# Kernel optimization log

Measured on AMD Instinct MI355X. Metric: run time of the kernel, lower is better.

## Reference

```python
import jax, jax.numpy as jnp
import numpy as np

N = 50000      # nodes
E = 800000     # edges
F = 500        # num_features
HID = 64       # hidden_channels
H = 4          # num_heads
HC = HID // H  # headc = 16
C = 8          # num_classes
KHOP = 2       # K hops
CST = 1e-5


def setup_inputs() -> dict:
    key = jax.random.key(0)
    ks = jax.random.split(key, 12)
    s = 0.02
    return {
        "node_feat": jax.random.normal(ks[0], (N, F), dtype=jnp.float32),
        "edge_index": jax.random.randint(ks[1], (2, E), 0, N, dtype=jnp.int64),
        "Wi": jax.random.normal(ks[2], (F, HID), dtype=jnp.float32) * s,
        "bi": jnp.zeros((HID,), dtype=jnp.float32),
        "Wq": jax.random.normal(ks[3], (HID, H * HC), dtype=jnp.float32) * s,
        "bq": jnp.zeros((H * HC,), dtype=jnp.float32),
        "Wk": jax.random.normal(ks[4], (HID, H * HC), dtype=jnp.float32) * s,
        "bk": jnp.zeros((H * HC,), dtype=jnp.float32),
        "Wv": jax.random.normal(ks[5], (HID, H * C), dtype=jnp.float32) * s,
        "bv": jnp.zeros((H * C,), dtype=jnp.float32),
        "Wo": jax.random.normal(ks[6], (H * C, C), dtype=jnp.float32) * s,
        "bo": jnp.zeros((C,), dtype=jnp.float32),
        "hopwise": jnp.ones((KHOP + 1,), dtype=jnp.float32),
        "headwise": jnp.zeros((H, KHOP), dtype=jnp.float32),
        "teleport": jnp.ones((1,), dtype=jnp.float32),
    }


def reference(node_feat, edge_index, Wi, bi, Wq, bq, Wk, bk, Wv, bv, Wo, bo,
              hopwise, headwise, teleport):
    row, col = edge_index[0], edge_index[1]
    # degree(col): in-degree; norm = deg^-1 indexed at row (as in the torch code)
    deg = jax.ops.segment_sum(jnp.ones((E,), dtype=node_feat.dtype), col,
                              num_segments=N)
    deg_inv = jnp.where(deg > 0, 1.0 / deg, 0.0)  # [N]

    x = jax.nn.relu(node_feat @ Wi + bi)          # dropout p=0.0 / eval -> identity
    Q = (1.0 + jax.nn.elu(x @ Wq + bq)).reshape(N, H, HC)
    Kf = (1.0 + jax.nn.elu(x @ Wk + bk)).reshape(N, H, HC)
    V = (x @ Wv + bv).reshape(N, H, C)

    M = jnp.einsum('nhi,nhj->nhij', Kf, V)        # [N,H,HC,C]
    hidden = V * hopwise[0]                       # ind_gamma & gamma_softmax
    layerwise = jax.nn.softmax(headwise, axis=0)  # softmax over heads (dim=-2)

    # global attention (teleport) term
    teleportM = jnp.sum(M, axis=0, keepdims=True) / N      # [1,H,HC,C]
    teleportK = jnp.sum(Kf, axis=0, keepdims=True) / N     # [1,H,HC]
    teleportH = jnp.einsum('nhi,bhij->nhj', Q, teleportM)  # [N,H,C]
    teleportC = jnp.einsum('nhi,bhi->nh', Q, teleportK)[..., None] + CST
    teleportH = (teleportH / teleportC).sum(axis=-2)       # [N,C]

    for hop in range(KHOP):
        # norm[e] = deg_inv[row[e]]  =>  pre-scale source nodes, then scatter-add
        M = jax.ops.segment_sum((M * deg_inv[:, None, None, None])[row], col,
                                num_segments=N)
        Kf = jax.ops.segment_sum((Kf * deg_inv[:, None, None])[row], col,
                                 num_segments=N)
        Hh = jnp.einsum('nhi,nhij->nhj', Q, M)             # [N,H,C]
        Cc = jnp.einsum('nhi,nhi->nh', Q, Kf)[..., None] + CST
        gamma = hopwise[hop + 1] * layerwise[:, hop][:, None]  # [H,1]
        hidden = hidden + gamma * (Hh / Cc)

    # multi_concat output projection
    hidden = hidden.reshape(N, H * C) @ Wo + bo
    return hidden + teleport * teleportH
```

## Files before the change

kernel.cpp:

```cpp
#include <hip/hip_runtime.h>
#include <hip/hip_bf16.h>
#include <stdint.h>
#include <stddef.h>

#define NN 50000
#define NE 800000
#define FIN 500
#define HIDN 64
#define NH 4
#define HCD 16
#define NC 8
#define KVROW 192
#define CSTF 1e-5f
#define SCAN_NB 196
#define XBLKS 3125

typedef float f32x2 __attribute__((ext_vector_type(2)));
typedef __attribute__((ext_vector_type(8))) short bf16x8;
typedef __attribute__((ext_vector_type(4))) float f32x4;

__device__ inline float bf_lo(unsigned u) {
    union { unsigned i; float f; } v; v.i = u << 16; return v.f;
}
__device__ inline f32x2 bfpair(unsigned u) {
    union { unsigned i; float f; } lo, hi;
    lo.i = u << 16; hi.i = u & 0xffff0000u;
    f32x2 r; r.x = lo.f; r.y = hi.f; return r;
}
__device__ inline unsigned short f2bf(float f) {
    union { float f; unsigned i; } v; v.f = f;
    unsigned r = v.i + 0x7fffu + ((v.i >> 16) & 1u);
    return (unsigned short)(r >> 16);
}
__device__ inline unsigned pack2bf(float a, float b) {
    __hip_bfloat162 h = __float22bfloat162_rn(make_float2(a, b));
    unsigned r; __builtin_memcpy(&r, &h, 4); return r;
}


__global__ void k_deg_wt(const int* __restrict__ col, int* __restrict__ deg,
                         const float* __restrict__ Wi, unsigned short* __restrict__ Wt) {
    int e = blockIdx.x * blockDim.x + threadIdx.x;
    if (e < NE) atomicAdd(&deg[col[e]], 1);
    if (e < 64 * 512) {
        int c = e >> 9;
        int k = e & 511;
        Wt[e] = (k < FIN) ? f2bf(Wi[(size_t)k * 64 + c]) : (unsigned short)0;
    }
}


__global__ void k_bsum(const int* __restrict__ deg, int* __restrict__ bsum,
                       float* __restrict__ dinv, int* __restrict__ cursor,
                       float* __restrict__ tMK) {
    __shared__ int red[256];
    int b = blockIdx.x, t = threadIdx.x;
    int i = b * 256 + t;
    int d = (i < NN) ? deg[i] : 0;
    if (i < NN) {
        dinv[i] = d > 0 ? 1.0f / (float)d : 0.0f;
        cursor[i] = 0;
    }
    if (b == 0)
        for (int j = t; j < 576; j += 256) tMK[j] = 0.f;
    red[t] = d;
    __syncthreads();
    for (int s = 128; s > 0; s >>= 1) {
        if (t < s) red[t] += red[t + s];
        __syncthreads();
    }
    if (t == 0) bsum[b] = red[0];
}

__global__ void k_bscan(const int* __restrict__ bsum, int* __restrict__ bex) {
    __shared__ int s[256];
    int t = threadIdx.x;
    int own = (t < SCAN_NB) ? bsum[t] : 0;
    s[t] = own;
    __syncthreads();
    for (int d = 1; d < 256; d <<= 1) {
        int v = (t >= d) ? s[t - d] : 0;
        __syncthreads();
        s[t] += v;
        __syncthreads();
    }
    if (t < SCAN_NB) bex[t] = s[t] - own;
}

__global__ void k_expand(const int* __restrict__ deg, const int* __restrict__ bex,
                         int* __restrict__ offs) {
    __shared__ int s[256];
    int b = blockIdx.x, t = threadIdx.x;
    int i = b * 256 + t;
    int v = (i < NN) ? deg[i] : 0;
    s[t] = v;
    __syncthreads();
    for (int d = 1; d < 256; d <<= 1) {
        int a = (t >= d) ? s[t - d] : 0;
        __syncthreads();
        s[t] += a;
        __syncthreads();
    }
    int excl = s[t] - v + bex[b];
    if (i < NN) offs[i] = excl;
    if (i == NN - 1) offs[NN] = excl + v;
}

__global__ void k_scatter(const int* __restrict__ row, const int* __restrict__ col,
                          const int* __restrict__ offs, int* __restrict__ cursor,
                          int* __restrict__ csr_src) {
    int e = blockIdx.x * blockDim.x + threadIdx.x;
    if (e < NE) {
        int c = col[e];
        int pos = offs[c] + atomicAdd(&cursor[c], 1);
        csr_src[pos] = row[e];
    }
}


__global__ __launch_bounds__(256) void k_xgemm(const float* __restrict__ nf,
                                               const unsigned short* __restrict__ Wt,
                                               const float* __restrict__ bi,
                                               float* __restrict__ x) {
    __shared__ __align__(16) float atile[16 * 516];
    int t = threadIdx.x;
    int lane = t & 63;
    int w = t >> 6;
    int quad = lane >> 4;
    int l15 = lane & 15;
    int n0 = blockIdx.x * 16;

#pragma unroll
    for (int i = 0; i < 4; i++) {
        int r = w * 4 + i;
        const float* rp = nf + (size_t)(n0 + r) * FIN;
        float4 v0 = *(const float4*)(rp + 4 * lane);
        int c1 = 256 + 4 * lane;
        int c1c = c1 > 496 ? 496 : c1;
        float4 v1 = *(const float4*)(rp + c1c);
        *(float4*)&atile[r * 516 + 4 * lane] = v0;
        *(float4*)&atile[r * 516 + c1] = v1;
    }
    __syncthreads();

    int kbase = w * 128;
    f32x4 acc[4];
#pragma unroll
    for (int ct = 0; ct < 4; ct++) acc[ct] = (f32x4){0.f, 0.f, 0.f, 0.f};

#pragma unroll
    for (int ks = 0; ks < 4; ks++) {
        int kk = kbase + ks * 32 + quad * 8;
        f32x4 fa = *(const f32x4*)&atile[l15 * 516 + kk];
        f32x4 fb = *(const f32x4*)&atile[l15 * 516 + kk + 4];
        union { unsigned u[4]; bf16x8 v; } A;
        A.u[0] = pack2bf(fa.x, fa.y); A.u[1] = pack2bf(fa.z, fa.w);
        A.u[2] = pack2bf(fb.x, fb.y); A.u[3] = pack2bf(fb.z, fb.w);
#pragma unroll
        for (int ct = 0; ct < 4; ct++) {
            bf16x8 b = *(const bf16x8*)&Wt[(size_t)(ct * 16 + l15) * 512 + kk];
            acc[ct] = __builtin_amdgcn_mfma_f32_16x16x32_bf16(A.v, b, acc[ct], 0, 0, 0);
        }
    }
    __syncthreads();

    float* red = atile;
#pragma unroll
    for (int ct = 0; ct < 4; ct++)
#pragma unroll
        for (int r = 0; r < 4; r++)
            red[(w * 16 + quad * 4 + r) * 68 + ct * 16 + l15] = acc[ct][r];
    __syncthreads();

    int ocol = t & 63;
    int orow0 = t >> 6;
    float bv = bi[ocol];
#pragma unroll
    for (int i = 0; i < 4; i++) {
        int orow = i * 4 + orow0;
        float s = red[(0 * 16 + orow) * 68 + ocol] + red[(1 * 16 + orow) * 68 + ocol]
                + red[(2 * 16 + orow) * 68 + ocol] + red[(3 * 16 + orow) * 68 + ocol];
        x[(size_t)(n0 + orow) * 64 + ocol] = fmaxf(s + bv, 0.f);
    }
}


__global__ __launch_bounds__(256) void k_qkv(const float* __restrict__ x,
    const float* __restrict__ Wq, const float* __restrict__ bq,
    const float* __restrict__ Wk, const float* __restrict__ bk,
    const float* __restrict__ Wv, const float* __restrict__ bv,
    const float* __restrict__ hopwise, const float* __restrict__ dinv,
    float* __restrict__ Qg, float* __restrict__ hid,
    unsigned char* __restrict__ kv0, float* __restrict__ tMK) {
    __shared__ float wq_s[64 * 64], wk_s[64 * 64], wv_s[64 * 32];
    __shared__ float bq_s[64], bk_s[64], bv_s[32];
    __shared__ float xs[4][8][64];
    __shared__ float tacc[576];
    int t = threadIdx.x;
    for (int i = t; i < 4096; i += 256) { wq_s[i] = Wq[i]; wk_s[i] = Wk[i]; }
    for (int i = t; i < 2048; i += 256) wv_s[i] = Wv[i];
    if (t < 64) { bq_s[t] = bq[t]; bk_s[t] = bk[t]; }
    if (t >= 64 && t < 96) bv_s[t - 64] = bv[t - 64];
    for (int i = t; i < 576; i += 256) tacc[i] = 0.f;
    __syncthreads();
    int lane = t & 63;
    int w = t >> 6;
    int h = lane >> 4;
    int vcol = lane & 31;
    float hw0 = hopwise[0];
    float tkp = 0.f;
    float tmp_[8];
#pragma unroll
    for (int j = 0; j < 8; j++) tmp_[j] = 0.f;
    int tiles = (NN + 31) >> 5;
    for (int tile = blockIdx.x; tile < tiles; tile += gridDim.x) {
        int n0 = tile * 32 + w * 8;
        __syncthreads();
#pragma unroll
        for (int u = 0; u < 8; u++) {
            int n = n0 + u;
            xs[w][u][lane] = (n < NN) ? x[(size_t)n * 64 + lane] : 0.f;
        }
        __syncthreads();
        float aq[8], ak[8], av[8];
#pragma unroll
        for (int u = 0; u < 8; u++) { aq[u] = 0.f; ak[u] = 0.f; av[u] = 0.f; }
        for (int f = 0; f < 64; f++) {
            float wqv = wq_s[f * 64 + lane];
            float wkv = wk_s[f * 64 + lane];
            float wvv = wv_s[f * 32 + vcol];
#pragma unroll
            for (int u = 0; u < 8; u++) {
                float xf = xs[w][u][f];
                aq[u] = fmaf(xf, wqv, aq[u]);
                ak[u] = fmaf(xf, wkv, ak[u]);
                av[u] = fmaf(xf, wvv, av[u]);
            }
        }
#pragma unroll
        for (int u = 0; u < 8; u++) {
            int n = n0 + u;
            float q = aq[u] + bq_s[lane];
            float k = ak[u] + bk_s[lane];
            float v = av[u] + bv_s[vcol];
            float Qv = q > 0.f ? 1.f + q : expf(q);
            float Kv = k > 0.f ? 1.f + k : expf(k);
            if (n < NN) {
                Qg[(size_t)n * 64 + lane] = Qv;
                float vj[8];
#pragma unroll
                for (int j = 0; j < 8; j++) vj[j] = __shfl(v, h * 8 + j, 64);
                tkp += Kv;
#pragma unroll
                for (int j = 0; j < 8; j++) tmp_[j] += Kv * vj[j];
                float dv = dinv[n];
                unsigned short* kvrow = (unsigned short*)(kv0 + (size_t)n * KVROW);
                kvrow[lane] = f2bf(Kv * dv);
                if (lane < 32) kvrow[64 + lane] = f2bf(v);
                if (lane < 32) hid[(size_t)n * 32 + lane] = v * hw0;
            }
        }
    }
#pragma unroll
    for (int j = 0; j < 8; j++) atomicAdd(&tacc[lane * 8 + j], tmp_[j]);
    atomicAdd(&tacc[512 + lane], tkp);
    __syncthreads();
    for (int i = t; i < 576; i += 256) atomicAdd(&tMK[i], tacc[i]);
}


__global__ __launch_bounds__(256) void k_hop0(const unsigned char* __restrict__ kv0,
    const int* __restrict__ offs, const int* __restrict__ csr_src,
    const float* __restrict__ dinv, const float* __restrict__ Qg,
    const float* __restrict__ hopwise, const float* __restrict__ headwise,
    unsigned char* __restrict__ Marr, unsigned char* __restrict__ Karr,
    float* __restrict__ hid) {
    int t = threadIdx.x;
    int lane = t & 63;
    int n = __builtin_amdgcn_readfirstlane((blockIdx.x * 256 + t) >> 6);
    if (n >= NN) return;
    int h = lane >> 4;
    float e0 = expf(headwise[0]);
    float e1 = expf(headwise[2]);
    float e2 = expf(headwise[4]);
    float e3 = expf(headwise[6]);
    float esum = e0 + e1 + e2 + e3;
    float eh = (h == 0) ? e0 : ((h == 1) ? e1 : ((h == 2) ? e2 : e3));
    float gam = hopwise[1] * eh / esum;

    int hoff = 128 + h * 16;
    int o0 = offs[n], o1 = offs[n + 1];
    float kacc = 0.f;
    f32x2 A0 = {0.f, 0.f}, A1 = {0.f, 0.f}, B0 = {0.f, 0.f}, B1 = {0.f, 0.f};
    int e = o0;
    for (; e + 7 < o1; e += 8) {
        float kk_[8]; uint4 vv[8];
#pragma unroll
        for (int q = 0; q < 8; q++) {
            int s = csr_src[e + q];
            const unsigned char* r = kv0 + (size_t)s * KVROW;
            kk_[q] = bf_lo(((const unsigned short*)r)[lane]);
            vv[q] = *(const uint4*)(r + hoff);
        }
#pragma unroll
        for (int q = 0; q < 8; q++) {
            float ka = kk_[q];
            f32x2 ka2; ka2.x = ka; ka2.y = ka;
            kacc += ka;
            A0 += ka2 * bfpair(vv[q].x);
            A1 += ka2 * bfpair(vv[q].y);
            B0 += ka2 * bfpair(vv[q].z);
            B1 += ka2 * bfpair(vv[q].w);
        }
    }
    for (; e < o1; e++) {
        int s = csr_src[e];
        const unsigned char* r = kv0 + (size_t)s * KVROW;
        float ka = bf_lo(((const unsigned short*)r)[lane]);
        uint4 va = *(const uint4*)(r + hoff);
        f32x2 ka2; ka2.x = ka; ka2.y = ka;
        kacc += ka;
        A0 += ka2 * bfpair(va.x);
        A1 += ka2 * bfpair(va.y);
        B0 += ka2 * bfpair(va.z);
        B1 += ka2 * bfpair(va.w);
    }
    {
        float dv = dinv[n];
        float s8 = dv * 8.f;
        float s16 = dv * 16.f;
        unsigned kb8 = __builtin_amdgcn_cvt_pk_fp8_f32(kacc * s8, 0.f, 0, false);
        Karr[(size_t)n * 64 + lane] = (unsigned char)(kb8 & 0xff);
        unsigned u0 = __builtin_amdgcn_cvt_pk_fp8_f32(A0.x * s16, A0.y * s16, 0, false);
        u0 = __builtin_amdgcn_cvt_pk_fp8_f32(A1.x * s16, A1.y * s16, u0, true);
        unsigned u1 = __builtin_amdgcn_cvt_pk_fp8_f32(B0.x * s16, B0.y * s16, 0, false);
        u1 = __builtin_amdgcn_cvt_pk_fp8_f32(B1.x * s16, B1.y * s16, u1, true);
        uint2 pv; pv.x = u0; pv.y = u1;
        *(uint2*)(Marr + (size_t)n * 512 + lane * 8) = pv;
    }
    float qv = Qg[(size_t)n * 64 + lane];
    float hh[8];
    hh[0] = qv * A0.x; hh[1] = qv * A0.y; hh[2] = qv * A1.x; hh[3] = qv * A1.y;
    hh[4] = qv * B0.x; hh[5] = qv * B0.y; hh[6] = qv * B1.x; hh[7] = qv * B1.y;
    float cc = qv * kacc;
#pragma unroll
    for (int s = 1; s < 16; s <<= 1) {
#pragma unroll
        for (int j = 0; j < 8; j++) hh[j] += __shfl_xor(hh[j], s, 16);
        cc += __shfl_xor(cc, s, 16);
    }
    if ((lane & 15) < 8) {
        int j = lane & 7;
        float val = j < 4 ? (j < 2 ? (j == 0 ? hh[0] : hh[1]) : (j == 2 ? hh[2] : hh[3]))
                          : (j < 6 ? (j == 4 ? hh[4] : hh[5]) : (j == 6 ? hh[6] : hh[7]));
        size_t idx = (size_t)n * 32 + h * 8 + j;
        hid[idx] += gam * val / (cc + CSTF);
    }
}


__global__ __launch_bounds__(256) void k_prop1(const unsigned char* __restrict__ Marr,
    const unsigned char* __restrict__ Karr,
    const int* __restrict__ offs, const int* __restrict__ csr_src,
    const float* __restrict__ Qg, const float* __restrict__ hopwise,
    const float* __restrict__ headwise, float* __restrict__ hid) {
    int t = threadIdx.x;
    int lane = t & 63;
    int n = __builtin_amdgcn_readfirstlane((blockIdx.x * 256 + t) >> 6);
    if (n >= NN) return;
    int h = lane >> 4;
    float e0 = expf(headwise[1]);
    float e1 = expf(headwise[3]);
    float e2 = expf(headwise[5]);
    float e3 = expf(headwise[7]);
    float esum = e0 + e1 + e2 + e3;
    float eh = (h == 0) ? e0 : ((h == 1) ? e1 : ((h == 2) ? e2 : e3));
    float gam = hopwise[2] * eh / esum * 0.0625f;

    int o0 = offs[n], o1 = offs[n + 1];
    float kacc = 0.f;
    f32x2 A0 = {0.f, 0.f}, A1 = {0.f, 0.f}, B0 = {0.f, 0.f}, B1 = {0.f, 0.f};
    int e = o0;
    for (; e + 7 < o1; e += 8) {
        unsigned kb[8]; uint2 mv[8];
#pragma unroll
        for (int q = 0; q < 8; q++) {
            int s = csr_src[e + q];
            kb[q] = Karr[(size_t)s * 64 + lane];
            mv[q] = *(const uint2*)(Marr + (size_t)s * 512 + lane * 8);
        }
#pragma unroll
        for (int q = 0; q < 8; q++) {
            f32x2 kv = __builtin_amdgcn_cvt_pk_f32_fp8(kb[q], false);
            kacc += kv.x;
            A0 += __builtin_amdgcn_cvt_pk_f32_fp8(mv[q].x, false);
            A1 += __builtin_amdgcn_cvt_pk_f32_fp8(mv[q].x, true);
            B0 += __builtin_amdgcn_cvt_pk_f32_fp8(mv[q].y, false);
            B1 += __builtin_amdgcn_cvt_pk_f32_fp8(mv[q].y, true);
        }
    }
    for (; e < o1; e++) {
        int s = csr_src[e];
        unsigned kb = Karr[(size_t)s * 64 + lane];
        uint2 mva = *(const uint2*)(Marr + (size_t)s * 512 + lane * 8);
        f32x2 kv = __builtin_amdgcn_cvt_pk_f32_fp8(kb, false);
        kacc += kv.x;
        A0 += __builtin_amdgcn_cvt_pk_f32_fp8(mva.x, false);
        A1 += __builtin_amdgcn_cvt_pk_f32_fp8(mva.x, true);
        B0 += __builtin_amdgcn_cvt_pk_f32_fp8(mva.y, false);
        B1 += __builtin_amdgcn_cvt_pk_f32_fp8(mva.y, true);
    }
    kacc *= 0.125f;
    float qv = Qg[(size_t)n * 64 + lane];
    float hh[8];
    hh[0] = qv * A0.x; hh[1] = qv * A0.y; hh[2] = qv * A1.x; hh[3] = qv * A1.y;
    hh[4] = qv * B0.x; hh[5] = qv * B0.y; hh[6] = qv * B1.x; hh[7] = qv * B1.y;
    float cc = qv * kacc;
#pragma unroll
    for (int s = 1; s < 16; s <<= 1) {
#pragma unroll
        for (int j = 0; j < 8; j++) hh[j] += __shfl_xor(hh[j], s, 16);
        cc += __shfl_xor(cc, s, 16);
    }
    if ((lane & 15) < 8) {
        int j = lane & 7;
        float val = j < 4 ? (j < 2 ? (j == 0 ? hh[0] : hh[1]) : (j == 2 ? hh[2] : hh[3]))
                          : (j < 6 ? (j == 4 ? hh[4] : hh[5]) : (j == 6 ? hh[6] : hh[7]));
        size_t idx = (size_t)n * 32 + h * 8 + j;
        hid[idx] += gam * val / (cc + CSTF);
    }
}


__global__ __launch_bounds__(256) void k_final(const float* __restrict__ hid,
    const float* __restrict__ Qg, const float* __restrict__ Wo,
    const float* __restrict__ bo, const float* __restrict__ tMK,
    const float* __restrict__ teleport, float* __restrict__ out) {
    __shared__ float tm[512];
    __shared__ float tk[64];
    __shared__ float wo[256];
    __shared__ float bos[8];
    int t = threadIdx.x;
    const float invN = 1.0f / (float)NN;
    for (int i = t; i < 512; i += 256) tm[i] = tMK[i] * invN;
    if (t < 64) tk[t] = tMK[512 + t] * invN;
    wo[t] = Wo[t & 255];
    if (t < 8) bos[t] = bo[t];
    __syncthreads();
    float tp = teleport[0];
    int lane = t & 63;
    int sub = lane & 7;
    int g = lane >> 3;
    int wid = (blockIdx.x * 256 + t) >> 6;
    int nwaves = gridDim.x * 4;
    for (int nb = wid * 8; nb < NN; nb += nwaves * 8) {
        int n = nb + g;
        if (n < NN) {
            const float* hrow = hid + (size_t)n * 32;
            const float* qrow = Qg + (size_t)n * 64;
            float o = bos[sub];
#pragma unroll
            for (int m = 0; m < 32; m++) o = fmaf(hrow[m], wo[m * 8 + sub], o);
            float th = 0.f;
#pragma unroll
            for (int h2 = 0; h2 < 4; h2++) {
                float num = 0.f, den = 0.f;
#pragma unroll
                for (int i = 0; i < 16; i++) {
                    float q = qrow[h2 * 16 + i];
                    num = fmaf(q, tm[h2 * 128 + i * 8 + sub], num);
                    den = fmaf(q, tk[h2 * 16 + i], den);
                }
                th += num / (den + CSTF);
            }
            out[(size_t)n * 8 + sub] = o + tp * th;
        }
    }
}


extern "C" void kernel_launch(void* const* d_in, const int* in_sizes, int n_in,
                              void* d_out, int out_size, void* d_ws, size_t ws_size,
                              hipStream_t stream) {
    const float* nf = (const float*)d_in[0];
    const int* ei = (const int*)d_in[1];
    const float* Wi = (const float*)d_in[2];
    const float* bi = (const float*)d_in[3];
    const float* Wq = (const float*)d_in[4];
    const float* bq = (const float*)d_in[5];
    const float* Wk = (const float*)d_in[6];
    const float* bk = (const float*)d_in[7];
    const float* Wv = (const float*)d_in[8];
    const float* bv = (const float*)d_in[9];
    const float* Wo = (const float*)d_in[10];
    const float* bo = (const float*)d_in[11];
    const float* hopwise = (const float*)d_in[12];
    const float* headwise = (const float*)d_in[13];
    const float* teleport = (const float*)d_in[14];
    float* out = (float*)d_out;

    char* base = (char*)d_ws;
    size_t off = 0;
    auto alloc = [&](size_t bytes) -> void* {
        void* p = base + off;
        off = (off + bytes + 255) & ~(size_t)255;
        return p;
    };
    int* deg = (int*)alloc(NN * 4);
    int* cursor = (int*)alloc(NN * 4);
    int* offs = (int*)alloc((NN + 1) * 4);
    int* bsum = (int*)alloc(256 * 4);
    int* bex = (int*)alloc(256 * 4);
    float* dinv = (float*)alloc(NN * 4);
    int* csr_src = (int*)alloc((size_t)NE * 4);
    unsigned short* Wt = (unsigned short*)alloc(64 * 512 * 2);
    float* xbuf = (float*)alloc((size_t)NN * 64 * 4);
    float* Qg = (float*)alloc((size_t)NN * 64 * 4);
    float* hid = (float*)alloc((size_t)NN * 32 * 4);
    unsigned char* kv0 = (unsigned char*)alloc((size_t)NN * KVROW);
    unsigned char* Marr = (unsigned char*)alloc((size_t)NN * 512);
    unsigned char* Karr = (unsigned char*)alloc((size_t)NN * 64);
    float* tMK = (float*)alloc(576 * 4);

    const int* rowp = ei;
    const int* colp = ei + NE;

    hipMemsetAsync(deg, 0, NN * 4, stream);

    k_deg_wt<<<(NE + 255) / 256, 256, 0, stream>>>(colp, deg, Wi, Wt);
    k_bsum<<<SCAN_NB, 256, 0, stream>>>(deg, bsum, dinv, cursor, tMK);
    k_bscan<<<1, 256, 0, stream>>>(bsum, bex);
    k_expand<<<SCAN_NB, 256, 0, stream>>>(deg, bex, offs);
    k_scatter<<<(NE + 255) / 256, 256, 0, stream>>>(rowp, colp, offs, cursor, csr_src);
    k_xgemm<<<XBLKS, 256, 0, stream>>>(nf, Wt, bi, xbuf);
    k_qkv<<<768, 256, 0, stream>>>(xbuf, Wq, bq, Wk, bk, Wv, bv, hopwise, dinv,
                                   Qg, hid, kv0, tMK);
    k_hop0<<<(NN * 64 + 255) / 256, 256, 0, stream>>>(kv0, offs, csr_src, dinv, Qg,
                                                      hopwise, headwise, Marr, Karr, hid);
    k_prop1<<<(NN * 64 + 255) / 256, 256, 0, stream>>>(Marr, Karr, offs, csr_src, Qg,
                                                       hopwise, headwise, hid);
    k_final<<<1563, 256, 0, stream>>>(hid, Qg, Wo, bo, tMK, teleport, out);
}
```

Before: 447.9 us.

## Fuse final projection and teleport term into second hop propagation kernel

The separate k_final kernel is removed. Its output projection (hidden @ Wo + bo) and the teleport attention term are now computed inside k_prop1 from the per-node values already in registers and shared memory, so the hid write-back and the re-read of hid and Q are gone. This saves one kernel launch and the extra memory traffic. In exchange every block loads the teleport and Wo tables into shared memory and needs extra shuffles and a barrier, and the early exit for out-of-range nodes was dropped. The k_qkv grid size also changes from 768 to 782.

```diff
diff --git a/kernel.cpp b/kernel.cpp
--- a/kernel.cpp
+++ b/kernel.cpp
@@ -363,11 +363,26 @@
     const unsigned char* __restrict__ Karr,
     const int* __restrict__ offs, const int* __restrict__ csr_src,
     const float* __restrict__ Qg, const float* __restrict__ hopwise,
-    const float* __restrict__ headwise, float* __restrict__ hid) {
+    const float* __restrict__ headwise, const float* __restrict__ hid,
+    const float* __restrict__ Wo, const float* __restrict__ bo,
+    const float* __restrict__ tMK, const float* __restrict__ teleport,
+    float* __restrict__ out) {
+    __shared__ float tm[512];
+    __shared__ float tk[64];
+    __shared__ float wo[256];
+    __shared__ float bos[8];
+    __shared__ float hrow[4][32];
     int t = threadIdx.x;
+    const float invN = 1.0f / (float)NN;
+    for (int i = t; i < 512; i += 256) tm[i] = tMK[i] * invN;
+    if (t < 64) tk[t] = tMK[512 + t] * invN;
+    wo[t] = Wo[t & 255];
+    if (t < 8) bos[t] = bo[t];
+    __syncthreads();
+
     int lane = t & 63;
+    int w = t >> 6;
     int n = __builtin_amdgcn_readfirstlane((blockIdx.x * 256 + t) >> 6);
-    if (n >= NN) return;
     int h = lane >> 4;
     float e0 = expf(headwise[1]);
     float e1 = expf(headwise[3]);
@@ -426,55 +441,39 @@
         int j = lane & 7;
         float val = j < 4 ? (j < 2 ? (j == 0 ? hh[0] : hh[1]) : (j == 2 ? hh[2] : hh[3]))
                           : (j < 6 ? (j == 4 ? hh[4] : hh[5]) : (j == 6 ? hh[6] : hh[7]));
-        size_t idx = (size_t)n * 32 + h * 8 + j;
-        hid[idx] += gam * val / (cc + CSTF);
-    }
-}
-
-
-__global__ __launch_bounds__(256) void k_final(const float* __restrict__ hid,
-    const float* __restrict__ Qg, const float* __restrict__ Wo,
-    const float* __restrict__ bo, const float* __restrict__ tMK,
-    const float* __restrict__ teleport, float* __restrict__ out) {
-    __shared__ float tm[512];
-    __shared__ float tk[64];
-    __shared__ float wo[256];
-    __shared__ float bos[8];
-    int t = threadIdx.x;
-    const float invN = 1.0f / (float)NN;
-    for (int i = t; i < 512; i += 256) tm[i] = tMK[i] * invN;
-    if (t < 64) tk[t] = tMK[512 + t] * invN;
-    wo[t] = Wo[t & 255];
-    if (t < 8) bos[t] = bo[t];
-    __syncthreads();
-    float tp = teleport[0];
-    int lane = t & 63;
-    int sub = lane & 7;
-    int g = lane >> 3;
-    int wid = (blockIdx.x * 256 + t) >> 6;
-    int nwaves = gridDim.x * 4;
-    for (int nb = wid * 8; nb < NN; nb += nwaves * 8) {
-        int n = nb + g;
-        if (n < NN) {
-            const float* hrow = hid + (size_t)n * 32;
-            const float* qrow = Qg + (size_t)n * 64;
-            float o = bos[sub];
-#pragma unroll
-            for (int m = 0; m < 32; m++) o = fmaf(hrow[m], wo[m * 8 + sub], o);
-            float th = 0.f;
-#pragma unroll
-            for (int h2 = 0; h2 < 4; h2++) {
-                float num = 0.f, den = 0.f;
-#pragma unroll
-                for (int i = 0; i < 16; i++) {
-                    float q = qrow[h2 * 16 + i];
-                    num = fmaf(q, tm[h2 * 128 + i * 8 + sub], num);
-                    den = fmaf(q, tk[h2 * 16 + i], den);
-                }
-                th += num / (den + CSTF);
-            }
-            out[(size_t)n * 8 + sub] = o + tp * th;
-        }
+        int m = h * 8 + j;
+        hrow[w][m] = hid[(size_t)n * 32 + m] + gam * val / (cc + CSTF);
+    }
+    const float* tml = &tm[lane * 8];
+    float nm[8];
+#pragma unroll
+    for (int s2 = 0; s2 < 8; s2++) nm[s2] = qv * tml[s2];
+    float dn = qv * tk[lane];
+#pragma unroll
+    for (int s = 1; s < 16; s <<= 1) {
+#pragma unroll
+        for (int s2 = 0; s2 < 8; s2++) nm[s2] += __shfl_xor(nm[s2], s, 64);
+        dn += __shfl_xor(dn, s, 64);
+    }
+    float ir = 1.0f / (dn + CSTF);
+#pragma unroll
+    for (int s2 = 0; s2 < 8; s2++) nm[s2] *= ir;
+#pragma unroll
+    for (int s2 = 0; s2 < 8; s2++) {
+        nm[s2] += __shfl_xor(nm[s2], 16, 64);
+        nm[s2] += __shfl_xor(nm[s2], 32, 64);
+    }
+    __syncthreads();
+    if (lane < 8) {
+        int sub = lane;
+        float th = sub < 4 ? (sub < 2 ? (sub == 0 ? nm[0] : nm[1])
+                                      : (sub == 2 ? nm[2] : nm[3]))
+                           : (sub < 6 ? (sub == 4 ? nm[4] : nm[5])
+                                      : (sub == 6 ? nm[6] : nm[7]));
+        float o = bos[sub];
+#pragma unroll
+        for (int m = 0; m < 32; m++) o = fmaf(hrow[w][m], wo[m * 8 + sub], o);
+        out[(size_t)n * 8 + sub] = o + teleport[0] * th;
     }
 }
 
@@ -533,11 +532,11 @@
     k_expand<<<SCAN_NB, 256, 0, stream>>>(deg, bex, offs);
     k_scatter<<<(NE + 255) / 256, 256, 0, stream>>>(rowp, colp, offs, cursor, csr_src);
     k_xgemm<<<XBLKS, 256, 0, stream>>>(nf, Wt, bi, xbuf);
-    k_qkv<<<768, 256, 0, stream>>>(xbuf, Wq, bq, Wk, bk, Wv, bv, hopwise, dinv,
+    k_qkv<<<782, 256, 0, stream>>>(xbuf, Wq, bq, Wk, bk, Wv, bv, hopwise, dinv,
                                    Qg, hid, kv0, tMK);
     k_hop0<<<(NN * 64 + 255) / 256, 256, 0, stream>>>(kv0, offs, csr_src, dinv, Qg,
                                                       hopwise, headwise, Marr, Karr, hid);
     k_prop1<<<(NN * 64 + 255) / 256, 256, 0, stream>>>(Marr, Karr, offs, csr_src, Qg,
-                                                       hopwise, headwise, hid);
-    k_final<<<1563, 256, 0, stream>>>(hid, Qg, Wo, bo, tMK, teleport, out);
-}
+                                                       hopwise, headwise, hid,
+                                                       Wo, bo, tMK, teleport, out);
+}
```

New measurement: 467.6 us. 1.04x slower.
